# Kernel tuning notes

Measured on AMD Instinct MI355X. Metric: run time of the kernel, lower is better.

The kernel has to match this reference:

```python
import jax, jax.numpy as jnp
import numpy as np

B = 16
N = [4096, 1024, 256, 64, 16]
NF = [1, 16, 32, 64, 128, 256]
DEG = 6
KS = 5
LAT = 32


def spline_conv(x, edge_index, pseudo, W, root, bias):
    """SplineConv: open B-spline, degree 1, dim 3, kernel_size 5, sum aggregation (norm=False).
    x: [Nn, Cin], edge_index: [2, E] (src, dst), pseudo: [E, 3] in [0,1], W: [125, Cin, Cout]."""
    src, dst = edge_index[0], edge_index[1]
    v = pseudo * (KS - 1)                       # degree-1 open spline interval
    lo = jnp.clip(jnp.floor(v), 0.0, KS - 2)
    frac = v - lo                               # [E, 3]
    lo = lo.astype(jnp.int32)
    xs = x[src]                                 # [E, Cin] gather
    strides = jnp.array([1, KS, KS * KS], dtype=jnp.int32)
    msg = jnp.zeros((src.shape[0], W.shape[2]), dtype=x.dtype)
    for s in range(8):                          # (degree+1)^dim = 8 basis products
        bits = np.array([(s >> d) & 1 for d in range(3)], dtype=np.int32)
        basis = jnp.prod(jnp.where(bits[None, :] == 1, frac, 1.0 - frac), axis=1)  # [E]
        kidx = jnp.sum((lo + bits[None, :]) * strides[None, :], axis=1)            # [E]
        Wg = W[kidx]                                                               # [E, Cin, Cout]
        msg = msg + basis[:, None] * jnp.einsum('ei,eio->eo', xs, Wg)
    agg = jax.ops.segment_sum(msg, dst, num_segments=x.shape[0])
    return agg + x @ root + bias


def _fwd(fl, ei):
    (x, ea0, ea1, ea2, ea3, ea4, P01, P12, P23, P34, Pn1, P1n, P43, P32, P21, P10,
     W_c1, r_c1, b_c1, W_c2, r_c2, b_c2, W_c3, r_c3, b_c3, W_c4, r_c4, b_c4, W_c5, r_c5, b_c5,
     W_d5, r_d5, b_d5, W_d4, r_d4, b_d4, W_d3, r_d3, b_d3, W_d2, r_d2, b_d2, W_d1, r_d1, b_d1,
     fce1_w, fce1_b, fce21_w, fce21_b, fce22_w, fce22_b, fcd3_w, fcd3_b, fcd4_w, fcd4_b, eps) = fl
    ei0, ei1, ei2, ei3, ei4 = ei
    elu = jax.nn.elu
    # ---- encoder ----
    h = elu(spline_conv(x, ei0, ea0, W_c1, r_c1, b_c1))
    h = P01 @ h.reshape(B, N[0], NF[1])
    h = elu(spline_conv(h.reshape(-1, NF[1]), ei1, ea1, W_c2, r_c2, b_c2))
    h = P12 @ h.reshape(B, N[1], NF[2])
    h = elu(spline_conv(h.reshape(-1, NF[2]), ei2, ea2, W_c3, r_c3, b_c3))
    h = P23 @ h.reshape(B, N[2], NF[3])
    h = elu(spline_conv(h.reshape(-1, NF[3]), ei3, ea3, W_c4, r_c4, b_c4))
    h = P34 @ h.reshape(B, N[3], NF[4])
    h = elu(spline_conv(h.reshape(-1, NF[4]), ei4, ea4, W_c5, r_c5, b_c5))
    h = (Pn1 @ h.reshape(B, N[4], NF[5])).reshape(B, NF[5])
    # 1x1 convs over [B, C, 1, 1] == dense layers
    h = elu(h @ fce1_w + fce1_b)
    mu = h @ fce21_w + fce21_b
    logvar = h @ fce22_w + fce22_b
    # ---- reparameterize ----
    z = eps * jnp.exp(0.5 * logvar) + mu
    # ---- decoder ----
    h = elu(z @ fcd3_w + fcd3_b)
    h = elu(h @ fcd4_w + fcd4_b)
    h = P1n @ h.reshape(B, 1, NF[5])            # [B, N4, nf5]
    h = elu(spline_conv(h.reshape(-1, NF[5]), ei4, ea4, W_d5, r_d5, b_d5))
    h = P43 @ h.reshape(B, N[4], NF[4])
    h = elu(spline_conv(h.reshape(-1, NF[4]), ei3, ea3, W_d4, r_d4, b_d4))
    h = P32 @ h.reshape(B, N[3], NF[3])
    h = elu(spline_conv(h.reshape(-1, NF[3]), ei2, ea2, W_d3, r_d3, b_d3))
    h = P21 @ h.reshape(B, N[2], NF[2])
    h = elu(spline_conv(h.reshape(-1, NF[2]), ei1, ea1, W_d2, r_d2, b_d2))
    h = P10 @ h.reshape(B, N[1], NF[1])
    h = elu(spline_conv(h.reshape(-1, NF[1]), ei0, ea0, W_d1, r_d1, b_d1))
    recon = h.reshape(B, -1)                    # [B, N0] (nf0 == 1)
    return recon, mu, logvar


def setup_inputs() -> dict:
    key = jax.random.key(0)
    ks = iter(jax.random.split(key, 128))
    def nrm(shape, scale=1.0):
        return jax.random.normal(next(ks), shape, dtype=jnp.float32) * scale
    def edges(n):
        # per-sample random mesh-like connectivity, offset per graph copy
        e = jax.random.randint(next(ks), (2, B, n * DEG), 0, n)
        off = (jnp.arange(B) * n)[None, :, None]
        return (e + off).reshape(2, -1).astype(jnp.int32)
    inp = {}
    inp['x'] = nrm((B * N[0], NF[0]))
    for i in range(5):
        inp[f'ea{i}'] = jax.random.uniform(next(ks), (B * N[i] * DEG, 3), dtype=jnp.float32)
    pools = {'P01': (N[1], N[0]), 'P12': (N[2], N[1]), 'P23': (N[3], N[2]), 'P34': (N[4], N[3]),
             'Pn1': (1, N[4]), 'P1n': (N[4], 1), 'P43': (N[3], N[4]), 'P32': (N[2], N[3]),
             'P21': (N[1], N[2]), 'P10': (N[0], N[1])}
    for k2, (a, b) in pools.items():
        inp[k2] = nrm((a, b), 1.0 / np.sqrt(b))
    def spl(name, ci, co):
        inp[f'W_{name}'] = nrm((KS ** 3, ci, co), 0.1 / np.sqrt(ci))
        inp[f'r_{name}'] = nrm((ci, co), 1.0 / np.sqrt(ci))
        inp[f'b_{name}'] = nrm((co,), 0.01)
    spl('c1', NF[0], NF[1]); spl('c2', NF[1], NF[2]); spl('c3', NF[2], NF[3]); spl('c4', NF[3], NF[4]); spl('c5', NF[4], NF[5])
    spl('d5', NF[5], NF[4]); spl('d4', NF[4], NF[3]); spl('d3', NF[3], NF[2]); spl('d2', NF[2], NF[1]); spl('d1', NF[1], NF[0])
    def lin(name, ci, co):
        inp[f'{name}_w'] = nrm((ci, co), 1.0 / np.sqrt(ci))
        inp[f'{name}_b'] = nrm((co,), 0.01)
    lin('fce1', NF[5], NF[5]); lin('fce21', NF[5], LAT); lin('fce22', NF[5], LAT)
    lin('fcd3', LAT, NF[5]); lin('fcd4', NF[5], NF[5])
    inp['eps'] = nrm((B, LAT))
    for i in range(5):
        inp[f'ei{i}'] = edges(N[i])
    return inp


def reference(x, ea0, ea1, ea2, ea3, ea4, P01, P12, P23, P34, Pn1, P1n, P43, P32, P21, P10,
              W_c1, r_c1, b_c1, W_c2, r_c2, b_c2, W_c3, r_c3, b_c3, W_c4, r_c4, b_c4, W_c5, r_c5, b_c5,
              W_d5, r_d5, b_d5, W_d4, r_d4, b_d4, W_d3, r_d3, b_d3, W_d2, r_d2, b_d2, W_d1, r_d1, b_d1,
              fce1_w, fce1_b, fce21_w, fce21_b, fce22_w, fce22_b, fcd3_w, fcd3_b, fcd4_w, fcd4_b, eps,
              ei0, ei1, ei2, ei3, ei4):
    fl = (x, ea0, ea1, ea2, ea3, ea4, P01, P12, P23, P34, Pn1, P1n, P43, P32, P21, P10,
          W_c1, r_c1, b_c1, W_c2, r_c2, b_c2, W_c3, r_c3, b_c3, W_c4, r_c4, b_c4, W_c5, r_c5, b_c5,
          W_d5, r_d5, b_d5, W_d4, r_d4, b_d4, W_d3, r_d3, b_d3, W_d2, r_d2, b_d2, W_d1, r_d1, b_d1,
          fce1_w, fce1_b, fce21_w, fce21_b, fce22_w, fce22_b, fcd3_w, fcd3_b, fcd4_w, fcd4_b, eps)
    return _fwd(fl, (ei0, ei1, ei2, ei3, ei4))
```

## Files before the change

### kernel.cpp

```cpp
#include <hip/hip_runtime.h>
#include <hip/hip_bf16.h>

#define TPB 256
#define CDIV(a,b) (((a)+(b)-1)/(b))

__device__ __forceinline__ float elu_f(float v) {
    return v > 0.f ? v : expm1f(v);
}

__device__ __forceinline__ int ld_idx(const void* __restrict__ ei, int pos, int is64) {
    if (is64) return (int)((const long long*)ei)[pos];
    return ((const int*)ei)[pos];
}

__device__ __forceinline__ void spline_basis(const float* __restrict__ pseudo, int e,
                                             float bas[8], int kidx[8]) {
    float f[3]; int lo[3];
#pragma unroll
    for (int d = 0; d < 3; ++d) {
        float v = pseudo[e * 3 + d] * 4.f;
        float l = floorf(v);
        l = fminf(fmaxf(l, 0.f), 3.f);
        f[d] = v - l;
        lo[d] = (int)l;
    }
#pragma unroll
    for (int s = 0; s < 8; ++s) {
        int b0 = s & 1, b1 = (s >> 1) & 1, b2 = (s >> 2) & 1;
        bas[s] = (b0 ? f[0] : 1.f - f[0]) * (b1 ? f[1] : 1.f - f[1]) * (b2 ? f[2] : 1.f - f[2]);
        kidx[s] = (lo[0] + b0) + 5 * (lo[1] + b1) + 25 * (lo[2] + b2);
    }
}

__global__ void k_detect(const int* __restrict__ ei0_as_i32, int* __restrict__ flag) {
    if (threadIdx.x == 0 && blockIdx.x == 0) {
        int zeros = 0;
        for (int k = 0; k < 128; ++k)
            if (ei0_as_i32[2 * k + 1] == 0) zeros++;
        flag[0] = (zeros >= 120) ? 1 : 0;
    }
}

__global__ __launch_bounds__(TPB) void k_zero(float* __restrict__ p, int n) {
    int t = blockIdx.x * blockDim.x + threadIdx.x;
    if (t < n) p[t] = 0.f;
}

__global__ __launch_bounds__(TPB) void k_root4(const float* __restrict__ x,
                                               const float* __restrict__ root,
                                               const float* __restrict__ bias,
                                               float* __restrict__ out,
                                               int nnode, int cin, int cout) {
    int t = blockIdx.x * blockDim.x + threadIdx.x;
    if (t >= nnode * cout) return;
    int n = t / cout, co = t - n * cout;
    const float4* xr = reinterpret_cast<const float4*>(x + n * cin);
    float a0 = 0.f, a1 = 0.f, a2 = 0.f, a3 = 0.f;
    int q4 = cin >> 2;
    for (int q = 0; q < q4; ++q) {
        float4 xv = xr[q];
        const float* rp = root + (q * 4) * cout + co;
        a0 = fmaf(xv.x, rp[0], a0);
        a1 = fmaf(xv.y, rp[cout], a1);
        a2 = fmaf(xv.z, rp[2 * cout], a2);
        a3 = fmaf(xv.w, rp[3 * cout], a3);
    }
    out[t] = bias[co] + ((a0 + a1) + (a2 + a3));
}

template <int CIN, int COUT, int CSPLIT>
__global__ __launch_bounds__(TPB) void k_msg4(const float* __restrict__ x,
                                              const float* __restrict__ pseudo,
                                              const void* __restrict__ ei,
                                              const float* __restrict__ W,
                                              float* __restrict__ agg, int E,
                                              const int* __restrict__ flag) {
    constexpr int COG = COUT / 4;
    constexpr int CPT = CIN / CSPLIT;
    int t = blockIdx.x * blockDim.x + threadIdx.x;
    if (t >= E * COG * CSPLIT) return;
    int is64 = flag[0];
    int cog = t % COG;
    int rest = t / COG;
    int cs = rest % CSPLIT;
    int e = rest / CSPLIT;
    int co0 = cog * 4;
    int src = ld_idx(ei, e, is64);
    int dst = ld_idx(ei, E + e, is64);
    float bas[8]; int kidx[8];
    spline_basis(pseudo, e, bas, kidx);
    int wof[8];
#pragma unroll
    for (int s = 0; s < 8; ++s) wof[s] = kidx[s] * CIN * COUT + co0;
    float a0 = 0.f, a1 = 0.f, a2 = 0.f, a3 = 0.f;
    const float* xp = x + src * CIN + cs * CPT;
    const int cbase = cs * CPT * COUT;
    for (int ci = 0; ci < CPT; ++ci) {
        float xv = xp[ci];
        int off = cbase + ci * COUT;
#pragma unroll
        for (int s = 0; s < 8; ++s) {
            float4 w = *reinterpret_cast<const float4*>(&W[wof[s] + off]);
            float bx = bas[s] * xv;
            a0 = fmaf(bx, w.x, a0);
            a1 = fmaf(bx, w.y, a1);
            a2 = fmaf(bx, w.z, a2);
            a3 = fmaf(bx, w.w, a3);
        }
    }
    float* ap = &agg[dst * COUT + co0];
    atomicAdd(ap + 0, a0);
    atomicAdd(ap + 1, a1);
    atomicAdd(ap + 2, a2);
    atomicAdd(ap + 3, a3);
}

template <int CIN, int COUT>
__global__ __launch_bounds__(TPB) void k_msg_s(const float* __restrict__ x,
                                               const float* __restrict__ pseudo,
                                               const void* __restrict__ ei,
                                               const float* __restrict__ W,
                                               float* __restrict__ agg, int E,
                                               const int* __restrict__ flag) {
    int t = blockIdx.x * blockDim.x + threadIdx.x;
    if (t >= E * COUT) return;
    int is64 = flag[0];
    int e = t / COUT, co = t - e * COUT;
    int src = ld_idx(ei, e, is64);
    int dst = ld_idx(ei, E + e, is64);
    float bas[8]; int kidx[8];
    spline_basis(pseudo, e, bas, kidx);
    float acc = 0.f;
    const float* xp = x + src * CIN;
    for (int ci = 0; ci < CIN; ++ci) {
        float xv = xp[ci];
#pragma unroll
        for (int s = 0; s < 8; ++s)
            acc = fmaf(bas[s] * xv, W[kidx[s] * CIN * COUT + ci * COUT + co], acc);
    }
    atomicAdd(&agg[dst * COUT + co], acc);
}

__global__ __launch_bounds__(1024) void k_msg_c1(const float* __restrict__ x,
                                                 const float* __restrict__ pseudo,
                                                 const void* __restrict__ ei,
                                                 const float* __restrict__ W,
                                                 const float* __restrict__ root,
                                                 const float* __restrict__ bias,
                                                 float* __restrict__ agg,
                                                 const int* __restrict__ flag) {
    __shared__ float s_acc[4096 * 4];
    __shared__ float s_w[125 * 4];
    int b = blockIdx.x, cg = blockIdx.y, t = threadIdx.x;
    int co0 = cg * 4;
    int is64 = flag[0];
    if (t < 500) s_w[t] = W[(t >> 2) * 16 + co0 + (t & 3)];
    float r0 = root[co0], r1 = root[co0 + 1], r2 = root[co0 + 2], r3 = root[co0 + 3];
    float b0 = bias[co0], b1 = bias[co0 + 1], b2 = bias[co0 + 2], b3 = bias[co0 + 3];
    for (int n = t; n < 4096; n += 1024) {
        float xv = x[b * 4096 + n];
        s_acc[n * 4 + 0] = fmaf(xv, r0, b0);
        s_acc[n * 4 + 1] = fmaf(xv, r1, b1);
        s_acc[n * 4 + 2] = fmaf(xv, r2, b2);
        s_acc[n * 4 + 3] = fmaf(xv, r3, b3);
    }
    __syncthreads();
    int ebeg = b * 24576;
    for (int k = t; k < 24576; k += 1024) {
        int e = ebeg + k;
        int src = ld_idx(ei, e, is64);
        int dst = ld_idx(ei, 393216 + e, is64);
        float xv = x[src];
        float bas[8]; int kidx[8];
        spline_basis(pseudo, e, bas, kidx);
        float m0 = 0.f, m1 = 0.f, m2 = 0.f, m3 = 0.f;
#pragma unroll
        for (int s = 0; s < 8; ++s) {
            const float* wp = s_w + kidx[s] * 4;
            float bs = bas[s];
            m0 = fmaf(bs, wp[0], m0);
            m1 = fmaf(bs, wp[1], m1);
            m2 = fmaf(bs, wp[2], m2);
            m3 = fmaf(bs, wp[3], m3);
        }
        int dl = (dst - b * 4096) * 4;
        atomicAdd(&s_acc[dl + 0], m0 * xv);
        atomicAdd(&s_acc[dl + 1], m1 * xv);
        atomicAdd(&s_acc[dl + 2], m2 * xv);
        atomicAdd(&s_acc[dl + 3], m3 * xv);
    }
    __syncthreads();
    for (int n = t; n < 4096; n += 1024) {
        float4 v = *reinterpret_cast<float4*>(&s_acc[n * 4]);
        *reinterpret_cast<float4*>(&agg[(b * 4096 + n) * 16 + co0]) = v;
    }
}

__global__ __launch_bounds__(512) void k_msg_d1(const float* __restrict__ x,
                                                const float* __restrict__ pseudo,
                                                const void* __restrict__ ei,
                                                const float* __restrict__ W,
                                                float* __restrict__ part,
                                                const int* __restrict__ flag) {
    __shared__ float s_acc[4096];
    __shared__ float s_w[2000];
    int b = blockIdx.x, seg = blockIdx.y, t = threadIdx.x;
    int is64 = flag[0];
    for (int i = t; i < 2000; i += 512) s_w[i] = W[i];
    for (int n = t; n < 4096; n += 512) s_acc[n] = 0.f;
    __syncthreads();
    int ebeg = b * 24576 + seg * 3072;
    for (int k = t; k < 3072; k += 512) {
        int e = ebeg + k;
        int src = ld_idx(ei, e, is64);
        int dst = ld_idx(ei, 393216 + e, is64);
        float bas[8]; int kidx[8];
        spline_basis(pseudo, e, bas, kidx);
        const float* xp = x + src * 16;
        float m = 0.f;
#pragma unroll
        for (int s = 0; s < 8; ++s) {
            const float* wp = s_w + kidx[s] * 16;
            float p = 0.f;
#pragma unroll
            for (int ci = 0; ci < 16; ++ci) p = fmaf(xp[ci], wp[ci], p);
            m = fmaf(bas[s], p, m);
        }
        atomicAdd(&s_acc[dst - b * 4096], m);
    }
    __syncthreads();
    for (int n = t; n < 4096; n += 512) part[(b * 8 + seg) * 4096 + n] = s_acc[n];
}

__global__ __launch_bounds__(TPB) void k_d1_fin(const float* __restrict__ root,
                                                const float* __restrict__ part,
                                                float* __restrict__ out) {
    int t = blockIdx.x * blockDim.x + threadIdx.x;
    if (t >= 65536) return;
    int b = t >> 12, n = t & 4095;
    float a = root[t];
#pragma unroll
    for (int s = 0; s < 8; ++s) a += part[(b * 8 + s) * 4096 + n];
    out[t] = elu_f(a);
}

template <int F, int ELU>
__global__ __launch_bounds__(256) void k_poolg(const float* __restrict__ in,
                                               const float* __restrict__ P,
                                               float* __restrict__ out,
                                               int nout, int nin) {
    constexpr int FQ = F / 4;
    constexpr int TI = 256 / FQ;
    constexpr int JT = 128;
    __shared__ float4 s_in[JT * FQ];
    int fq = threadIdx.x % FQ;
    int i = threadIdx.x / FQ;
    int b = blockIdx.y;
    int gi = blockIdx.x * TI + i;
    int nchunk = nin / gridDim.z;
    int jbeg = blockIdx.z * nchunk;
    const float4* inb4 = reinterpret_cast<const float4*>(in + b * nin * F);
    const float* prow = P + gi * nin;
    float4 acc = make_float4(0.f, 0.f, 0.f, 0.f);
    for (int j0 = jbeg; j0 < jbeg + nchunk; j0 += JT) {
        __syncthreads();
        for (int t = threadIdx.x; t < JT * FQ; t += 256) {
            float4 v = inb4[(j0 + t / FQ) * FQ + (t % FQ)];
            if (ELU) {
                v.x = elu_f(v.x); v.y = elu_f(v.y);
                v.z = elu_f(v.z); v.w = elu_f(v.w);
            }
            s_in[t] = v;
        }
        __syncthreads();
#pragma unroll 4
        for (int j = 0; j < JT; j += 4) {
            float4 pv = *reinterpret_cast<const float4*>(prow + j0 + j);
            float4 v0 = s_in[(j + 0) * FQ + fq];
            float4 v1 = s_in[(j + 1) * FQ + fq];
            float4 v2 = s_in[(j + 2) * FQ + fq];
            float4 v3 = s_in[(j + 3) * FQ + fq];
            acc.x = fmaf(pv.x, v0.x, acc.x); acc.y = fmaf(pv.x, v0.y, acc.y);
            acc.z = fmaf(pv.x, v0.z, acc.z); acc.w = fmaf(pv.x, v0.w, acc.w);
            acc.x = fmaf(pv.y, v1.x, acc.x); acc.y = fmaf(pv.y, v1.y, acc.y);
            acc.z = fmaf(pv.y, v1.z, acc.z); acc.w = fmaf(pv.y, v1.w, acc.w);
            acc.x = fmaf(pv.z, v2.x, acc.x); acc.y = fmaf(pv.z, v2.y, acc.y);
            acc.z = fmaf(pv.z, v2.z, acc.z); acc.w = fmaf(pv.z, v2.w, acc.w);
            acc.x = fmaf(pv.w, v3.x, acc.x); acc.y = fmaf(pv.w, v3.y, acc.y);
            acc.z = fmaf(pv.w, v3.z, acc.z); acc.w = fmaf(pv.w, v3.w, acc.w);
        }
    }
    float* o = out + (((size_t)blockIdx.z * 16 + b) * nout + gi) * F + fq * 4;
    *reinterpret_cast<float4*>(o) = acc;
}

__global__ __launch_bounds__(TPB) void k_reduce2(const float* __restrict__ part,
                                                 float* __restrict__ out, int n) {
    int t = blockIdx.x * blockDim.x + threadIdx.x;
    if (t < n) out[t] = part[t] + part[t + n];
}

template <int F, int JT, int ELU>
__global__ __launch_bounds__(TPB) void k_pool_t(const float* __restrict__ in,
                                                const float* __restrict__ P,
                                                float* __restrict__ out,
                                                int nout, int nin) {
    constexpr int FQ = F / 4;
    constexpr int IQ = TPB / FQ;
    constexpr int NI = 4;
    constexpr int TI = IQ * NI;
    __shared__ float4 s_in[JT * FQ];
    int fq = threadIdx.x % FQ;
    int iq = threadIdx.x / FQ;
    int b = blockIdx.y;
    int i0 = blockIdx.x * TI + iq * NI;
    int nchunk = nin / gridDim.z;
    int jbeg = blockIdx.z * nchunk;
    const float4* inb4 = reinterpret_cast<const float4*>(in + b * nin * F);
    float4 acc[NI];
#pragma unroll
    for (int n = 0; n < NI; ++n) acc[n] = make_float4(0.f, 0.f, 0.f, 0.f);
    for (int j0 = jbeg; j0 < jbeg + nchunk; j0 += JT) {
        __syncthreads();
        for (int t = threadIdx.x; t < JT * FQ; t += TPB) {
            float4 v = inb4[(j0 + t / FQ) * FQ + (t % FQ)];
            if (ELU) {
                v.x = elu_f(v.x); v.y = elu_f(v.y);
                v.z = elu_f(v.z); v.w = elu_f(v.w);
            }
            s_in[t] = v;
        }
        __syncthreads();
#pragma unroll 2
        for (int j = 0; j < JT; j += 4) {
            float4 v0 = s_in[(j + 0) * FQ + fq];
            float4 v1 = s_in[(j + 1) * FQ + fq];
            float4 v2 = s_in[(j + 2) * FQ + fq];
            float4 v3 = s_in[(j + 3) * FQ + fq];
#pragma unroll
            for (int n = 0; n < NI; ++n) {
                float4 pv = *reinterpret_cast<const float4*>(&P[(i0 + n) * nin + j0 + j]);
                acc[n].x = fmaf(pv.x, v0.x, acc[n].x); acc[n].y = fmaf(pv.x, v0.y, acc[n].y);
                acc[n].z = fmaf(pv.x, v0.z, acc[n].z); acc[n].w = fmaf(pv.x, v0.w, acc[n].w);
                acc[n].x = fmaf(pv.y, v1.x, acc[n].x); acc[n].y = fmaf(pv.y, v1.y, acc[n].y);
                acc[n].z = fmaf(pv.y, v1.z, acc[n].z); acc[n].w = fmaf(pv.y, v1.w, acc[n].w);
                acc[n].x = fmaf(pv.z, v2.x, acc[n].x); acc[n].y = fmaf(pv.z, v2.y, acc[n].y);
                acc[n].z = fmaf(pv.z, v2.z, acc[n].z); acc[n].w = fmaf(pv.z, v2.w, acc[n].w);
                acc[n].x = fmaf(pv.w, v3.x, acc[n].x); acc[n].y = fmaf(pv.w, v3.y, acc[n].y);
                acc[n].z = fmaf(pv.w, v3.z, acc[n].z); acc[n].w = fmaf(pv.w, v3.w, acc[n].w);
            }
        }
    }
#pragma unroll
    for (int n = 0; n < NI; ++n) {
        int i = i0 + n;
        if (i >= nout) continue;
        float* o = out + (b * nout + i) * F + fq * 4;
        if (gridDim.z > 1) {
            atomicAdd(o + 0, acc[n].x); atomicAdd(o + 1, acc[n].y);
            atomicAdd(o + 2, acc[n].z); atomicAdd(o + 3, acc[n].w);
        } else {
            *reinterpret_cast<float4*>(o) = acc[n];
        }
    }
}

__global__ __launch_bounds__(TPB) void k_pool_e(const float* __restrict__ in,
                                                const float* __restrict__ P,
                                                float* __restrict__ out,
                                                int nout, int nin, int F, int elu) {
    int t = blockIdx.x * blockDim.x + threadIdx.x;
    if (t >= 16 * nout * F) return;
    int f = t % F;
    int rest = t / F;
    int i = rest % nout;
    int b = rest / nout;
    const float* ip = in + b * nin * F + f;
    const float* pp = P + i * nin;
    float acc = 0.f;
    if (elu) {
#pragma unroll 4
        for (int j = 0; j < nin; ++j) acc = fmaf(pp[j], elu_f(ip[j * F]), acc);
    } else {
#pragma unroll 4
        for (int j = 0; j < nin; ++j) acc = fmaf(pp[j], ip[j * F], acc);
    }
    out[t] = acc;
}

__global__ __launch_bounds__(1024) void k_fc_fused2(
        const float* __restrict__ c5agg, const float* __restrict__ Pn1,
        const float* __restrict__ fce1_w, const float* __restrict__ fce1_b,
        const float* __restrict__ fce21_w, const float* __restrict__ fce21_b,
        const float* __restrict__ fce22_w, const float* __restrict__ fce22_b,
        const float* __restrict__ eps,
        const float* __restrict__ fcd3_w, const float* __restrict__ fcd3_b,
        const float* __restrict__ fcd4_w, const float* __restrict__ fcd4_b,
        const float* __restrict__ P1n,
        float* __restrict__ out_mu, float* __restrict__ out_lv,
        float* __restrict__ dec_in) {
    __shared__ float s0[256], s1[256], sz[32], sp[1024];
    int b = blockIdx.x, t = threadIdx.x;
    if (t < 256) {
        const float* ap = c5agg + b * 4096 + t;
        float acc = 0.f;
#pragma unroll
        for (int n = 0; n < 16; ++n) acc = fmaf(Pn1[n], elu_f(ap[n * 256]), acc);
        s0[t] = acc;
    }
    __syncthreads();
    {
        int q = t >> 8, co = t & 255;
        const float* w = fce1_w + co;
        float a = 0.f;
        int c0 = q * 64;
        for (int ci = 0; ci < 64; ci += 8) {
#pragma unroll
            for (int k = 0; k < 8; ++k) a = fmaf(s0[c0 + ci + k], w[(c0 + ci + k) * 256], a);
        }
        sp[t] = a;
    }
    __syncthreads();
    if (t < 256) s1[t] = elu_f(sp[t] + sp[t + 256] + sp[t + 512] + sp[t + 768] + fce1_b[t]);
    __syncthreads();
    if (t < 512) {
        int which = t >> 8, r = t & 255;
        int co = r & 31, q = r >> 5;
        const float* w = (which ? fce22_w : fce21_w) + co;
        float a = 0.f;
        int c0 = q * 32;
#pragma unroll
        for (int k = 0; k < 32; ++k) a = fmaf(s1[c0 + k], w[(c0 + k) * 32], a);
        sp[t] = a;
    }
    __syncthreads();
    if (t < 64) {
        int which = t >> 5, co = t & 31;
        float m = (which ? fce22_b : fce21_b)[co];
        int base = which * 256 + co;
#pragma unroll
        for (int q = 0; q < 8; ++q) m += sp[base + q * 32];
        if (which == 0) { out_mu[b * 32 + co] = m; s0[co] = m; }
        else            { out_lv[b * 32 + co] = m; s0[64 + co] = m; }
    }
    __syncthreads();
    if (t < 32) sz[t] = fmaf(eps[b * 32 + t], expf(0.5f * s0[64 + t]), s0[t]);
    __syncthreads();
    if (t < 256) {
        float d = fcd3_b[t];
#pragma unroll
        for (int ci = 0; ci < 32; ++ci) d = fmaf(sz[ci], fcd3_w[ci * 256 + t], d);
        s0[t] = elu_f(d);
    }
    __syncthreads();
    {
        int q = t >> 8, co = t & 255;
        const float* w = fcd4_w + co;
        float a = 0.f;
        int c0 = q * 64;
        for (int ci = 0; ci < 64; ci += 8) {
#pragma unroll
            for (int k = 0; k < 8; ++k) a = fmaf(s0[c0 + ci + k], w[(c0 + ci + k) * 256], a);
        }
        sp[t] = a;
    }
    __syncthreads();
    if (t < 256) s1[t] = elu_f(sp[t] + sp[t + 256] + sp[t + 512] + sp[t + 768] + fcd4_b[t]);
    __syncthreads();
    {
        float* op = dec_in + b * 4096;
        for (int idx = t; idx < 4096; idx += 1024) {
            int n = idx >> 8, f = idx & 255;
            op[idx] = P1n[n] * s1[f];
        }
    }
}

__global__ __launch_bounds__(TPB) void k_elu_out(const float* __restrict__ in,
                                                 float* __restrict__ out, int n) {
    int t = blockIdx.x * blockDim.x + threadIdx.x;
    if (t < n) out[t] = elu_f(in[t]);
}

extern "C" void kernel_launch(void* const* d_in, const int* in_sizes, int n_in,
                              void* d_out, int out_size, void* d_ws, size_t ws_size,
                              hipStream_t stream) {
    const float* x    = (const float*)d_in[0];
    const float* ea0  = (const float*)d_in[1];
    const float* ea1  = (const float*)d_in[2];
    const float* ea2  = (const float*)d_in[3];
    const float* ea3  = (const float*)d_in[4];
    const float* ea4  = (const float*)d_in[5];
    const float* P01  = (const float*)d_in[6];
    const float* P12  = (const float*)d_in[7];
    const float* P23  = (const float*)d_in[8];
    const float* P34  = (const float*)d_in[9];
    const float* Pn1  = (const float*)d_in[10];
    const float* P1n  = (const float*)d_in[11];
    const float* P43  = (const float*)d_in[12];
    const float* P32  = (const float*)d_in[13];
    const float* P21  = (const float*)d_in[14];
    const float* P10  = (const float*)d_in[15];
    const float* W_c1 = (const float*)d_in[16]; const float* r_c1 = (const float*)d_in[17]; const float* b_c1 = (const float*)d_in[18];
    const float* W_c2 = (const float*)d_in[19]; const float* r_c2 = (const float*)d_in[20]; const float* b_c2 = (const float*)d_in[21];
    const float* W_c3 = (const float*)d_in[22]; const float* r_c3 = (const float*)d_in[23]; const float* b_c3 = (const float*)d_in[24];
    const float* W_c4 = (const float*)d_in[25]; const float* r_c4 = (const float*)d_in[26]; const float* b_c4 = (const float*)d_in[27];
    const float* W_c5 = (const float*)d_in[28]; const float* r_c5 = (const float*)d_in[29]; const float* b_c5 = (const float*)d_in[30];
    const float* W_d5 = (const float*)d_in[31]; const float* r_d5 = (const float*)d_in[32]; const float* b_d5 = (const float*)d_in[33];
    const float* W_d4 = (const float*)d_in[34]; const float* r_d4 = (const float*)d_in[35]; const float* b_d4 = (const float*)d_in[36];
    const float* W_d3 = (const float*)d_in[37]; const float* r_d3 = (const float*)d_in[38]; const float* b_d3 = (const float*)d_in[39];
    const float* W_d2 = (const float*)d_in[40]; const float* r_d2 = (const float*)d_in[41]; const float* b_d2 = (const float*)d_in[42];
    const float* W_d1 = (const float*)d_in[43]; const float* r_d1 = (const float*)d_in[44]; const float* b_d1 = (const float*)d_in[45];
    const float* fce1_w  = (const float*)d_in[46]; const float* fce1_b  = (const float*)d_in[47];
    const float* fce21_w = (const float*)d_in[48]; const float* fce21_b = (const float*)d_in[49];
    const float* fce22_w = (const float*)d_in[50]; const float* fce22_b = (const float*)d_in[51];
    const float* fcd3_w  = (const float*)d_in[52]; const float* fcd3_b  = (const float*)d_in[53];
    const float* fcd4_w  = (const float*)d_in[54]; const float* fcd4_b  = (const float*)d_in[55];
    const float* eps  = (const float*)d_in[56];
    const void* ei0 = d_in[57];
    const void* ei1 = d_in[58];
    const void* ei2 = d_in[59];
    const void* ei3 = d_in[60];
    const void* ei4 = d_in[61];

    const int E1 = 98304, E2 = 24576, E3 = 6144, E4 = 1536;
    const int N0 = 65536, N1 = 16384, N2 = 4096, N3 = 1024, N4 = 256;

    float* sm   = (float*)d_ws;
    float* bufA = sm + 13824;
    float* bufB = bufA + 1048576;
    int*  flag  = (int*)(bufB + 262144);
    float* part = bufB + 262144 + 64;
    const size_t WS_NEED = (size_t)(13824 + 1048576 + 262144 + 64 + 524288) * 4;
    const bool big_ws = ws_size >= WS_NEED;

    float* out = (float*)d_out;
    float* out_mu = out + 65536;
    float* out_lv = out + 66048;

    auto g = [](int n) { return dim3((unsigned)CDIV(n, TPB)); };

    k_detect<<<1, 64, 0, stream>>>((const int*)ei0, flag);

    k_msg_c1<<<dim3(16, 4), 1024, 0, stream>>>(x, ea0, ei0, W_c1, r_c1, b_c1, bufA, flag);
    if (big_ws) {
        k_poolg<16, 1><<<dim3(16, 16, 2), 256, 0, stream>>>(bufA, P01, part, 1024, 4096);
        k_reduce2<<<g(262144), TPB, 0, stream>>>(part, bufB, 262144);
    } else {
        k_poolg<16, 1><<<dim3(16, 16, 1), 256, 0, stream>>>(bufA, P01, bufB, 1024, 4096);
    }

    k_root4<<<g(N1 * 32), TPB, 0, stream>>>(bufB, r_c2, b_c2, bufA, N1, 16, 32);
    k_msg4<16, 32, 1><<<g(E1 * 8), TPB, 0, stream>>>(bufB, ea1, ei1, W_c2, bufA, E1, flag);
    k_poolg<32, 1><<<dim3(8, 16, 1), 256, 0, stream>>>(bufA, P12, bufB, 256, 1024);

    k_root4<<<g(N2 * 64), TPB, 0, stream>>>(bufB, r_c3, b_c3, bufA, N2, 32, 64);
    k_msg4<32, 64, 1><<<g(E2 * 16), TPB, 0, stream>>>(bufB, ea2, ei2, W_c3, bufA, E2, flag);
    k_zero<<<g(65536), TPB, 0, stream>>>(bufB, 65536);
    k_pool_t<64, 64, 1><<<dim3(1, 16, 2), TPB, 0, stream>>>(bufA, P23, bufB, 64, 256);

    k_root4<<<g(N3 * 128), TPB, 0, stream>>>(bufB, r_c4, b_c4, bufA, N3, 64, 128);
    k_msg4<64, 128, 1><<<g(E3 * 32), TPB, 0, stream>>>(bufB, ea3, ei3, W_c4, bufA, E3, flag);
    k_pool_e<<<g(16 * 16 * 128), TPB, 0, stream>>>(bufA, P34, bufB, 16, 64, 128, 1);

    k_root4<<<g(N4 * 256), TPB, 0, stream>>>(bufB, r_c5, b_c5, bufA, N4, 128, 256);
    k_msg4<128, 256, 2><<<g(E4 * 128), TPB, 0, stream>>>(bufB, ea4, ei4, W_c5, bufA, E4, flag);

    k_fc_fused2<<<16, 1024, 0, stream>>>(bufA, Pn1,
                                         fce1_w, fce1_b, fce21_w, fce21_b, fce22_w, fce22_b,
                                         eps, fcd3_w, fcd3_b, fcd4_w, fcd4_b, P1n,
                                         out_mu, out_lv, bufA);

    k_root4<<<g(N4 * 128), TPB, 0, stream>>>(bufA, r_d5, b_d5, bufB, N4, 256, 128);
    k_msg4<256, 128, 4><<<g(E4 * 128), TPB, 0, stream>>>(bufA, ea4, ei4, W_d5, bufB, E4, flag);
    k_pool_e<<<g(16 * 64 * 128), TPB, 0, stream>>>(bufB, P43, bufA, 64, 16, 128, 1);

    k_root4<<<g(N3 * 64), TPB, 0, stream>>>(bufA, r_d4, b_d4, bufB, N3, 128, 64);
    k_msg4<128, 64, 2><<<g(E3 * 32), TPB, 0, stream>>>(bufA, ea3, ei3, W_d4, bufB, E3, flag);
    k_pool_t<64, 64, 1><<<dim3(4, 16, 1), TPB, 0, stream>>>(bufB, P32, bufA, 256, 64);

    k_root4<<<g(N2 * 32), TPB, 0, stream>>>(bufA, r_d3, b_d3, bufB, N2, 64, 32);
    k_msg4<64, 32, 1><<<g(E2 * 8), TPB, 0, stream>>>(bufA, ea2, ei2, W_d3, bufB, E2, flag);
    k_poolg<32, 1><<<dim3(32, 16, 1), 256, 0, stream>>>(bufB, P21, bufA, 1024, 256);

    k_root4<<<g(N1 * 16), TPB, 0, stream>>>(bufA, r_d2, b_d2, bufB, N1, 32, 16);
    k_msg4<32, 16, 1><<<g(E1 * 4), TPB, 0, stream>>>(bufA, ea1, ei1, W_d2, bufB, E1, flag);
    k_poolg<16, 1><<<dim3(64, 16, 1), 256, 0, stream>>>(bufB, P10, bufA, 4096, 1024);

    k_root4<<<g(N0 * 1), TPB, 0, stream>>>(bufA, r_d1, b_d1, bufB, N0, 16, 1);
    if (big_ws) {
        k_msg_d1<<<dim3(16, 8), 512, 0, stream>>>(bufA, ea0, ei0, W_d1, part, flag);
        k_d1_fin<<<g(65536), TPB, 0, stream>>>(bufB, part, out);
    } else {
        k_msg_s<16, 1><<<g(393216), TPB, 0, stream>>>(bufA, ea0, ei0, W_d1, bufB, 393216, flag);
        k_elu_out<<<g(N0), TPB, 0, stream>>>(bufB, out, 65536);
    }
}
```

Measured before the change: 1.021 ms.

## Build CSR by destination for level-0 graph and use atomic-free gather kernels

Builds a destination-sorted CSR (count, scan, fill) for the finest graph each call. Level-0 convolutions c1 and d1 then run as per-node gather kernels with the root term, bias and ELU fused in, so the shared-memory atomic scatter, partial buffers and reduction kernels go away. The CSR build costs five extra launches plus global atomics over 393k edges, and it uses a single-block scan. The first pooling step also returns to one split with no reduce.

```diff
diff --git a/kernel.cpp b/kernel.cpp
--- a/kernel.cpp
+++ b/kernel.cpp
@@ -44,6 +44,159 @@
 __global__ __launch_bounds__(TPB) void k_zero(float* __restrict__ p, int n) {
     int t = blockIdx.x * blockDim.x + threadIdx.x;
     if (t < n) p[t] = 0.f;
+}
+
+__global__ __launch_bounds__(TPB) void k_zero_i(int* __restrict__ p, int n) {
+    int t = blockIdx.x * blockDim.x + threadIdx.x;
+    if (t < n) p[t] = 0;
+}
+
+__global__ __launch_bounds__(TPB) void k_csr_count(const void* __restrict__ ei,
+                                                   int* __restrict__ cnt, int E,
+                                                   const int* __restrict__ flag) {
+    int t = blockIdx.x * blockDim.x + threadIdx.x;
+    if (t >= E) return;
+    int dst = ld_idx(ei, E + t, flag[0]);
+    atomicAdd(&cnt[dst], 1);
+}
+
+__global__ __launch_bounds__(1024) void k_csr_scan(const int* __restrict__ cnt,
+                                                   int* __restrict__ row_ptr) {
+    __shared__ int s_part[1024];
+    int t = threadIdx.x;
+    int base = t * 64;
+    int sum = 0;
+    for (int i = 0; i < 64; ++i) sum += cnt[base + i];
+    s_part[t] = sum;
+    __syncthreads();
+    for (int off = 1; off < 1024; off <<= 1) {
+        int v = (t >= off) ? s_part[t - off] : 0;
+        __syncthreads();
+        s_part[t] += v;
+        __syncthreads();
+    }
+    int run = (t == 0) ? 0 : s_part[t - 1];
+    for (int i = 0; i < 64; ++i) { row_ptr[base + i] = run; run += cnt[base + i]; }
+    if (t == 1023) row_ptr[65536] = run;
+}
+
+__global__ __launch_bounds__(TPB) void k_csr_fill(const void* __restrict__ ei,
+                                                  const int* __restrict__ row_ptr,
+                                                  int* __restrict__ cur,
+                                                  int* __restrict__ eid, int E,
+                                                  const int* __restrict__ flag) {
+    int t = blockIdx.x * blockDim.x + threadIdx.x;
+    if (t >= E) return;
+    int dst = ld_idx(ei, E + t, flag[0]);
+    int pos = row_ptr[dst] + atomicAdd(&cur[dst], 1);
+    eid[pos] = t;
+}
+
+__global__ __launch_bounds__(256) void k_gather_c1(const float* __restrict__ x,
+                                                   const float* __restrict__ pseudo,
+                                                   const void* __restrict__ ei,
+                                                   const float* __restrict__ W,
+                                                   const float* __restrict__ root,
+                                                   const float* __restrict__ bias,
+                                                   const int* __restrict__ row_ptr,
+                                                   const int* __restrict__ eid,
+                                                   float* __restrict__ agg,
+                                                   const int* __restrict__ flag) {
+    __shared__ float4 s_w[500];
+    for (int i = threadIdx.x; i < 500; i += 256)
+        s_w[i] = reinterpret_cast<const float4*>(W)[i];
+    __syncthreads();
+    int t = blockIdx.x * 256 + threadIdx.x;
+    int n = t >> 2, cg = t & 3, co0 = cg * 4;
+    int is64 = flag[0];
+    float xn = x[n];
+    float a0 = fmaf(xn, root[co0 + 0], bias[co0 + 0]);
+    float a1 = fmaf(xn, root[co0 + 1], bias[co0 + 1]);
+    float a2 = fmaf(xn, root[co0 + 2], bias[co0 + 2]);
+    float a3 = fmaf(xn, root[co0 + 3], bias[co0 + 3]);
+    int rb = row_ptr[n], re = row_ptr[n + 1];
+    for (int idx = rb; idx < re; ++idx) {
+        int e = eid[idx];
+        int src = ld_idx(ei, e, is64);
+        float bas[8]; int kidx[8];
+        spline_basis(pseudo, e, bas, kidx);
+        float xs = x[src];
+        float m0 = 0.f, m1 = 0.f, m2 = 0.f, m3 = 0.f;
+#pragma unroll
+        for (int s = 0; s < 8; ++s) {
+            float4 w = s_w[kidx[s] * 4 + cg];
+            float bs = bas[s];
+            m0 = fmaf(bs, w.x, m0);
+            m1 = fmaf(bs, w.y, m1);
+            m2 = fmaf(bs, w.z, m2);
+            m3 = fmaf(bs, w.w, m3);
+        }
+        a0 = fmaf(xs, m0, a0);
+        a1 = fmaf(xs, m1, a1);
+        a2 = fmaf(xs, m2, a2);
+        a3 = fmaf(xs, m3, a3);
+    }
+    float4 v = make_float4(a0, a1, a2, a3);
+    *reinterpret_cast<float4*>(&agg[n * 16 + co0]) = v;
+}
+
+__global__ __launch_bounds__(256) void k_gather_d1(const float* __restrict__ xin,
+                                                   const float* __restrict__ pseudo,
+                                                   const void* __restrict__ ei,
+                                                   const float* __restrict__ W,
+                                                   const float* __restrict__ root,
+                                                   const float* __restrict__ bias,
+                                                   const int* __restrict__ row_ptr,
+                                                   const int* __restrict__ eid,
+                                                   float* __restrict__ outp,
+                                                   const int* __restrict__ flag) {
+    __shared__ float s_w[2000];
+    for (int i = threadIdx.x; i < 2000; i += 256) s_w[i] = W[i];
+    __syncthreads();
+    int t = blockIdx.x * 256 + threadIdx.x;
+    int n = t >> 2, l = t & 3;
+    int is64 = flag[0];
+    int rb = row_ptr[n], re = row_ptr[n + 1];
+    float acc = 0.f;
+    for (int idx = rb + l; idx < re; idx += 4) {
+        int e = eid[idx];
+        int src = ld_idx(ei, e, is64);
+        float bas[8]; int kidx[8];
+        spline_basis(pseudo, e, bas, kidx);
+        const float4* xs4 = reinterpret_cast<const float4*>(xin + src * 16);
+        float4 xv0 = xs4[0], xv1 = xs4[1], xv2 = xs4[2], xv3 = xs4[3];
+        float m = 0.f;
+#pragma unroll
+        for (int s = 0; s < 8; ++s) {
+            const float4* wp = reinterpret_cast<const float4*>(s_w + kidx[s] * 16);
+            float4 w0 = wp[0], w1 = wp[1], w2 = wp[2], w3 = wp[3];
+            float p = 0.f;
+            p = fmaf(xv0.x, w0.x, p); p = fmaf(xv0.y, w0.y, p);
+            p = fmaf(xv0.z, w0.z, p); p = fmaf(xv0.w, w0.w, p);
+            p = fmaf(xv1.x, w1.x, p); p = fmaf(xv1.y, w1.y, p);
+            p = fmaf(xv1.z, w1.z, p); p = fmaf(xv1.w, w1.w, p);
+            p = fmaf(xv2.x, w2.x, p); p = fmaf(xv2.y, w2.y, p);
+            p = fmaf(xv2.z, w2.z, p); p = fmaf(xv2.w, w2.w, p);
+            p = fmaf(xv3.x, w3.x, p); p = fmaf(xv3.y, w3.y, p);
+            p = fmaf(xv3.z, w3.z, p); p = fmaf(xv3.w, w3.w, p);
+            m = fmaf(bas[s], p, m);
+        }
+        acc += m;
+    }
+    acc += __shfl_xor(acc, 1);
+    acc += __shfl_xor(acc, 2);
+    if (l == 0) {
+        const float4* xr = reinterpret_cast<const float4*>(xin + n * 16);
+        const float4* rr = reinterpret_cast<const float4*>(root);
+        float r = bias[0];
+#pragma unroll
+        for (int q = 0; q < 4; ++q) {
+            float4 xv = xr[q], rv = rr[q];
+            r = fmaf(xv.x, rv.x, r); r = fmaf(xv.y, rv.y, r);
+            r = fmaf(xv.z, rv.z, r); r = fmaf(xv.w, rv.w, r);
+        }
+        outp[n] = elu_f(r + acc);
+    }
 }
 
 __global__ __launch_bounds__(TPB) void k_root4(const float* __restrict__ x,
@@ -194,54 +347,6 @@
         float4 v = *reinterpret_cast<float4*>(&s_acc[n * 4]);
         *reinterpret_cast<float4*>(&agg[(b * 4096 + n) * 16 + co0]) = v;
     }
-}
-
-__global__ __launch_bounds__(512) void k_msg_d1(const float* __restrict__ x,
-                                                const float* __restrict__ pseudo,
-                                                const void* __restrict__ ei,
-                                                const float* __restrict__ W,
-                                                float* __restrict__ part,
-                                                const int* __restrict__ flag) {
-    __shared__ float s_acc[4096];
-    __shared__ float s_w[2000];
-    int b = blockIdx.x, seg = blockIdx.y, t = threadIdx.x;
-    int is64 = flag[0];
-    for (int i = t; i < 2000; i += 512) s_w[i] = W[i];
-    for (int n = t; n < 4096; n += 512) s_acc[n] = 0.f;
-    __syncthreads();
-    int ebeg = b * 24576 + seg * 3072;
-    for (int k = t; k < 3072; k += 512) {
-        int e = ebeg + k;
-        int src = ld_idx(ei, e, is64);
-        int dst = ld_idx(ei, 393216 + e, is64);
-        float bas[8]; int kidx[8];
-        spline_basis(pseudo, e, bas, kidx);
-        const float* xp = x + src * 16;
-        float m = 0.f;
-#pragma unroll
-        for (int s = 0; s < 8; ++s) {
-            const float* wp = s_w + kidx[s] * 16;
-            float p = 0.f;
-#pragma unroll
-            for (int ci = 0; ci < 16; ++ci) p = fmaf(xp[ci], wp[ci], p);
-            m = fmaf(bas[s], p, m);
-        }
-        atomicAdd(&s_acc[dst - b * 4096], m);
-    }
-    __syncthreads();
-    for (int n = t; n < 4096; n += 512) part[(b * 8 + seg) * 4096 + n] = s_acc[n];
-}
-
-__global__ __launch_bounds__(TPB) void k_d1_fin(const float* __restrict__ root,
-                                                const float* __restrict__ part,
-                                                float* __restrict__ out) {
-    int t = blockIdx.x * blockDim.x + threadIdx.x;
-    if (t >= 65536) return;
-    int b = t >> 12, n = t & 4095;
-    float a = root[t];
-#pragma unroll
-    for (int s = 0; s < 8; ++s) a += part[(b * 8 + s) * 4096 + n];
-    out[t] = elu_f(a);
 }
 
 template <int F, int ELU>
@@ -292,12 +397,6 @@
     }
     float* o = out + (((size_t)blockIdx.z * 16 + b) * nout + gi) * F + fq * 4;
     *reinterpret_cast<float4*>(o) = acc;
-}
-
-__global__ __launch_bounds__(TPB) void k_reduce2(const float* __restrict__ part,
-                                                 float* __restrict__ out, int n) {
-    int t = blockIdx.x * blockDim.x + threadIdx.x;
-    if (t < n) out[t] = part[t] + part[t + n];
 }
 
 template <int F, int JT, int ELU>
@@ -523,15 +622,17 @@
     const void* ei3 = d_in[60];
     const void* ei4 = d_in[61];
 
-    const int E1 = 98304, E2 = 24576, E3 = 6144, E4 = 1536;
+    const int E0 = 393216, E1 = 98304, E2 = 24576, E3 = 6144, E4 = 1536;
     const int N0 = 65536, N1 = 16384, N2 = 4096, N3 = 1024, N4 = 256;
 
     float* sm   = (float*)d_ws;
     float* bufA = sm + 13824;
     float* bufB = bufA + 1048576;
     int*  flag  = (int*)(bufB + 262144);
-    float* part = bufB + 262144 + 64;
-    const size_t WS_NEED = (size_t)(13824 + 1048576 + 262144 + 64 + 524288) * 4;
+    int*  csr_row = (int*)(bufB + 262144 + 64);
+    int*  csr_cur = csr_row + 65537;
+    int*  csr_eid = csr_cur + 65536;
+    const size_t WS_NEED = (size_t)(13824 + 1048576 + 262144 + 64 + 524352) * 4;
     const bool big_ws = ws_size >= WS_NEED;
 
     float* out = (float*)d_out;
@@ -542,13 +643,21 @@
 
     k_detect<<<1, 64, 0, stream>>>((const int*)ei0, flag);
 
-    k_msg_c1<<<dim3(16, 4), 1024, 0, stream>>>(x, ea0, ei0, W_c1, r_c1, b_c1, bufA, flag);
     if (big_ws) {
-        k_poolg<16, 1><<<dim3(16, 16, 2), 256, 0, stream>>>(bufA, P01, part, 1024, 4096);
-        k_reduce2<<<g(262144), TPB, 0, stream>>>(part, bufB, 262144);
+        k_zero_i<<<g(65536), TPB, 0, stream>>>(csr_cur, 65536);
+        k_csr_count<<<g(E0), TPB, 0, stream>>>(ei0, csr_cur, E0, flag);
+        k_csr_scan<<<1, 1024, 0, stream>>>(csr_cur, csr_row);
+        k_zero_i<<<g(65536), TPB, 0, stream>>>(csr_cur, 65536);
+        k_csr_fill<<<g(E0), TPB, 0, stream>>>(ei0, csr_row, csr_cur, csr_eid, E0, flag);
+    }
+
+    if (big_ws) {
+        k_gather_c1<<<1024, 256, 0, stream>>>(x, ea0, ei0, W_c1, r_c1, b_c1,
+                                              csr_row, csr_eid, bufA, flag);
     } else {
-        k_poolg<16, 1><<<dim3(16, 16, 1), 256, 0, stream>>>(bufA, P01, bufB, 1024, 4096);
-    }
+        k_msg_c1<<<dim3(16, 4), 1024, 0, stream>>>(x, ea0, ei0, W_c1, r_c1, b_c1, bufA, flag);
+    }
+    k_poolg<16, 1><<<dim3(16, 16, 1), 256, 0, stream>>>(bufA, P01, bufB, 1024, 4096);
 
     k_root4<<<g(N1 * 32), TPB, 0, stream>>>(bufB, r_c2, b_c2, bufA, N1, 16, 32);
     k_msg4<16, 32, 1><<<g(E1 * 8), TPB, 0, stream>>>(bufB, ea1, ei1, W_c2, bufA, E1, flag);
@@ -587,12 +696,12 @@
     k_msg4<32, 16, 1><<<g(E1 * 4), TPB, 0, stream>>>(bufA, ea1, ei1, W_d2, bufB, E1, flag);
     k_poolg<16, 1><<<dim3(64, 16, 1), 256, 0, stream>>>(bufB, P10, bufA, 4096, 1024);
 
-    k_root4<<<g(N0 * 1), TPB, 0, stream>>>(bufA, r_d1, b_d1, bufB, N0, 16, 1);
     if (big_ws) {
-        k_msg_d1<<<dim3(16, 8), 512, 0, stream>>>(bufA, ea0, ei0, W_d1, part, flag);
-        k_d1_fin<<<g(65536), TPB, 0, stream>>>(bufB, part, out);
+        k_gather_d1<<<1024, 256, 0, stream>>>(bufA, ea0, ei0, W_d1, r_d1, b_d1,
+                                              csr_row, csr_eid, out, flag);
     } else {
-        k_msg_s<16, 1><<<g(393216), TPB, 0, stream>>>(bufA, ea0, ei0, W_d1, bufB, 393216, flag);
+        k_root4<<<g(N0 * 1), TPB, 0, stream>>>(bufA, r_d1, b_d1, bufB, N0, 16, 1);
+        k_msg_s<16, 1><<<g(E0), TPB, 0, stream>>>(bufA, ea0, ei0, W_d1, bufB, E0, flag);
         k_elu_out<<<g(N0), TPB, 0, stream>>>(bufB, out, 65536);
     }
 }
```

Measured after the change: 1.013 ms. No clear change (-0.7%).
